# Optimization experiments

Hardware: AMD Instinct MI355X
Metric: run time of the kernel (lower is better)

Reference implementation:

```python
import jax, jax.numpy as jnp
import numpy as np

B, T, D, UNITS, NUM_OUT = 64, 1024, 256, 256, 32


def setup_inputs() -> dict:
    key = jax.random.key(0)
    k1, k2, k3 = jax.random.split(key, 3)
    inputs = jax.random.normal(k1, (B, T, D), dtype=jnp.float32)
    U = jax.random.normal(k2, (D, 4 * UNITS), dtype=jnp.float32) * 0.05
    W = jax.random.normal(k3, (UNITS, 4 * UNITS), dtype=jnp.float32) * 0.05
    b = jnp.zeros((4 * UNITS,), dtype=jnp.float32)
    return {"inputs": inputs, "U": U, "W": W, "b": b, "num_outputs": NUM_OUT}


def reference(inputs, U, W, b, num_outputs):
    # inputs: [B, T, D]; U: [D, 4u]; W: [u, 4u]; b: [4u]
    Bsz, Tlen, _ = inputs.shape
    units = W.shape[0]
    # Precompute input projection as one batched GEMM (x_t @ U + b for all t)
    xz = jnp.einsum('btd,dk->btk', inputs, U) + b  # [B, T, 4u]

    def step(carry, xz_t):
        h, c = carry
        z = xz_t + h @ W  # [B, 4u]
        z0, z1, z2, z3 = jnp.split(z, 4, axis=1)
        i = jax.nn.sigmoid(z0)
        f = jax.nn.sigmoid(z1)
        c_new = f * c + i * jnp.tanh(z2)
        o = jax.nn.sigmoid(z3)
        h_new = o * jnp.tanh(c_new)
        return (h_new, c_new), h_new

    h0 = jnp.zeros((Bsz, units), dtype=inputs.dtype)
    c0 = jnp.zeros((Bsz, units), dtype=inputs.dtype)
    (_, _), hs = jax.lax.scan(step, (h0, c0), jnp.swapaxes(xz, 0, 1))  # hs: [T, B, u]
    outputs = jnp.swapaxes(hs, 0, 1)[:, Tlen - num_outputs:, :]  # [B, num_outputs, u]
    return outputs
```

## Files before the change

kernel.cpp:

```cpp
#include <hip/hip_runtime.h>
#include <hip/hip_fp16.h>
#include <stdint.h>

#define Bsz 64
#define Tsz 1024
#define Dsz 256
#define UNITSn 256
#define Zdim 1024

typedef _Float16 f16x8  __attribute__((ext_vector_type(8)));
typedef float    f32x4  __attribute__((ext_vector_type(4)));

__device__ __forceinline__ float dot2acc(uint32_t w, uint32_t h, float acc) {
  asm("v_dot2_f32_f16 %0, %1, %2, %0" : "+v"(acc) : "v"(w), "v"(h));
  return acc;
}

__device__ __forceinline__ float dot4(const uint4& w, const uint4& h, float acc) {
  acc = dot2acc(w.x, h.x, acc); acc = dot2acc(w.y, h.y, acc);
  acc = dot2acc(w.z, h.z, acc); acc = dot2acc(w.w, h.w, acc);
  return acc;
}

__device__ __forceinline__ float sigm(float x)   { return 1.0f / (1.0f + __expf(-x)); }
__device__ __forceinline__ float tanh_f(float x) { return 1.0f - 2.0f / (__expf(2.0f * x) + 1.0f); }

__global__ __launch_bounds__(256) void convert_u(const float* __restrict__ U,
                                                 _Float16* __restrict__ UT) {
  int i = blockIdx.x * 256 + threadIdx.x;
  int n = i >> 8, k = i & 255;
  UT[i] = (_Float16)U[(size_t)k * Zdim + n];
}

__global__ __launch_bounds__(256) void convert_w7(const float* __restrict__ W,
                                                  uint4* __restrict__ Wop,
                                                  uint4* __restrict__ Wlds,
                                                  uint4* __restrict__ Wstr) {
  int i = blockIdx.x * 256 + threadIdx.x;
  if (i >= 32768) return;
  int slot = i >> 9, t = i & 511;
  int g, jx, outIdx;
  uint4* dst;
  if (slot < 40)      { g = slot / 10;      jx = slot % 10;        dst = Wop;  outIdx = slot * 512 + t; }
  else if (slot < 52) { int ss = slot - 40; g = ss & 3; jx = 10 + (ss >> 2); dst = Wlds; outIdx = ss * 512 + t; }
  else                { int ss = slot - 52; g = ss & 3; jx = 13 + (ss >> 2); dst = Wstr; outIdx = ss * 512 + t; }
  int col = g * 256 + (t & 255);
  int kbase = (t >> 8) * 64 + jx * 4;
  uint32_t d[4];
#pragma unroll
  for (int e = 0; e < 4; e++) {
    int k2 = kbase + e;
    float w0 = W[(size_t)(2 * k2) * Zdim + col];
    float w1 = W[(size_t)(2 * k2 + 1) * Zdim + col];
    __half2 p = __floats2half2_rn(w0, w1);
    d[e] = __builtin_bit_cast(uint32_t, p);
  }
  dst[outIdx] = make_uint4(d[0], d[1], d[2], d[3]);
}

__global__ __launch_bounds__(256) void proj_mfma(
    const float* __restrict__ x, const _Float16* __restrict__ UT,
    const float* __restrict__ bias, float* __restrict__ xz, int t0) {
  __shared__ _Float16 Ax[64][40];
  __shared__ _Float16 Ux[256][40];
  const int tid  = threadIdx.x;
  const int w    = tid >> 6, lane = tid & 63;
  const int lr   = lane & 15, kg = lane >> 4;
  const int n0   = blockIdx.x * 256;
  const int tloc = blockIdx.y;
  const int t    = t0 + tloc;
  const int arow = tid >> 2, ak = (tid & 3) * 8;

  f32x4 acc[4][4];
#pragma unroll
  for (int mi = 0; mi < 4; mi++)
#pragma unroll
    for (int ni = 0; ni < 4; ni++) acc[mi][ni] = f32x4{0.f, 0.f, 0.f, 0.f};

  for (int k0 = 0; k0 < Dsz; k0 += 32) {
    const float* xp = x + ((size_t)arow * Tsz + t) * Dsz + k0 + ak;
    float4 p0 = *(const float4*)xp;
    float4 p1 = *(const float4*)(xp + 4);
    const _Float16* up = UT + (size_t)(n0 + tid) * Dsz + k0;
    f16x8 u0 = *(const f16x8*)up;
    f16x8 u1 = *(const f16x8*)(up + 8);
    f16x8 u2 = *(const f16x8*)(up + 16);
    f16x8 u3 = *(const f16x8*)(up + 24);
    __syncthreads();
    f16x8 a8;
    a8[0] = (_Float16)p0.x; a8[1] = (_Float16)p0.y;
    a8[2] = (_Float16)p0.z; a8[3] = (_Float16)p0.w;
    a8[4] = (_Float16)p1.x; a8[5] = (_Float16)p1.y;
    a8[6] = (_Float16)p1.z; a8[7] = (_Float16)p1.w;
    *(f16x8*)&Ax[arow][ak] = a8;
    *(f16x8*)&Ux[tid][0]  = u0;
    *(f16x8*)&Ux[tid][8]  = u1;
    *(f16x8*)&Ux[tid][16] = u2;
    *(f16x8*)&Ux[tid][24] = u3;
    __syncthreads();
    f16x8 af[4], uf[4];
#pragma unroll
    for (int mi = 0; mi < 4; mi++) af[mi] = *(const f16x8*)&Ax[mi * 16 + lr][kg * 8];
#pragma unroll
    for (int ni = 0; ni < 4; ni++) uf[ni] = *(const f16x8*)&Ux[w * 64 + ni * 16 + lr][kg * 8];
#pragma unroll
    for (int mi = 0; mi < 4; mi++)
#pragma unroll
      for (int ni = 0; ni < 4; ni++)
        acc[mi][ni] = __builtin_amdgcn_mfma_f32_16x16x32_f16(af[mi], uf[ni],
                                                             acc[mi][ni], 0, 0, 0);
  }
#pragma unroll
  for (int ni = 0; ni < 4; ni++) {
    int col = n0 + w * 64 + ni * 16 + lr;
    float bs = bias[col];
#pragma unroll
    for (int mi = 0; mi < 4; mi++) {
      f32x4 v = acc[mi][ni];
#pragma unroll
      for (int r = 0; r < 4; r++) {
        int brow = mi * 16 + kg * 4 + r;
        xz[((size_t)tloc * 64 + brow) * Zdim + col] = v[r] + bs;
      }
    }
  }
}

__global__ __launch_bounds__(512) void lstm_chunk(
    const float* __restrict__ xz, const uint4* __restrict__ Wop,
    const uint4* __restrict__ WldsBuf, const uint4* __restrict__ Wstr,
    float* __restrict__ out, uint4* __restrict__ h_state,
    float* __restrict__ c_state, int t0, int Tc, int n_out) {
  __shared__ uint4 Wl[12 * 512];
  __shared__ uint4 hq[2][32];
  __shared__ float4 pp[256];

  const int tid  = threadIdx.x;
  const int b    = blockIdx.x;
  const int half = tid >> 8, u = tid & 255;

  uint4 wop[40];
#pragma unroll
  for (int j = 0; j < 40; j++) wop[j] = Wop[(size_t)j * 512 + tid];
#pragma unroll
  for (int j = 0; j < 40; j++)
    asm volatile("" : "+v"(wop[j].x), "+v"(wop[j].y), "+v"(wop[j].z), "+v"(wop[j].w));
#pragma unroll
  for (int cl = 0; cl < 12; cl++)
    Wl[(size_t)cl * 512 + tid] = WldsBuf[(size_t)cl * 512 + tid];

  float c = 0.0f;
  if (t0 == 0) {
    if (tid < 64) ((uint4*)hq)[tid] = make_uint4(0, 0, 0, 0);
  } else {
    if (tid < 32) ((uint4*)hq)[tid] = h_state[(size_t)b * 32 + tid];
    if (half == 0) c = c_state[(size_t)b * 256 + u];
  }
  __syncthreads();

  const float* xzb = xz + (size_t)b * Zdim + u;
  float nx0 = 0, nx1 = 0, nx2 = 0, nx3 = 0;
  if (half == 0) { nx0 = xzb[0]; nx1 = xzb[256]; nx2 = xzb[512]; nx3 = xzb[768]; }
  const uint4* wstr = Wstr + tid;

  for (int tl = 0; tl < Tc; tl++) {
    const int buf = tl & 1;
    const uint4* hb = hq[buf] + half * 16;
    float a0 = 0, a1 = 0, a2 = 0, a3 = 0;

    uint4 s00 = wstr[0 * 512], s01 = wstr[1 * 512], s02 = wstr[2 * 512], s03 = wstr[3 * 512];
    uint4 s10 = wstr[4 * 512], s11 = wstr[5 * 512], s12 = wstr[6 * 512], s13 = wstr[7 * 512];

#pragma unroll
    for (int j = 0; j < 10; j++) {
      uint4 h4 = hb[j];
      a0 = dot4(wop[0 * 10 + j], h4, a0);
      a1 = dot4(wop[1 * 10 + j], h4, a1);
      a2 = dot4(wop[2 * 10 + j], h4, a2);
      a3 = dot4(wop[3 * 10 + j], h4, a3);
    }
    uint4 s20, s21, s22, s23;
    { uint4 h4 = hb[13];
      s20 = wstr[8 * 512]; s21 = wstr[9 * 512]; s22 = wstr[10 * 512]; s23 = wstr[11 * 512];
      a0 = dot4(s00, h4, a0); a1 = dot4(s01, h4, a1);
      a2 = dot4(s02, h4, a2); a3 = dot4(s03, h4, a3); }
    { uint4 h4 = hb[10];
      uint4 w0 = Wl[(size_t)0 * 512 + tid], w1 = Wl[(size_t)1 * 512 + tid];
      uint4 w2 = Wl[(size_t)2 * 512 + tid], w3 = Wl[(size_t)3 * 512 + tid];
      a0 = dot4(w0, h4, a0); a1 = dot4(w1, h4, a1);
      a2 = dot4(w2, h4, a2); a3 = dot4(w3, h4, a3); }
    { uint4 h4 = hb[14];
      a0 = dot4(s10, h4, a0); a1 = dot4(s11, h4, a1);
      a2 = dot4(s12, h4, a2); a3 = dot4(s13, h4, a3); }
    { uint4 h4 = hb[11];
      uint4 w0 = Wl[(size_t)4 * 512 + tid], w1 = Wl[(size_t)5 * 512 + tid];
      uint4 w2 = Wl[(size_t)6 * 512 + tid], w3 = Wl[(size_t)7 * 512 + tid];
      a0 = dot4(w0, h4, a0); a1 = dot4(w1, h4, a1);
      a2 = dot4(w2, h4, a2); a3 = dot4(w3, h4, a3); }
    { uint4 h4 = hb[15];
      a0 = dot4(s20, h4, a0); a1 = dot4(s21, h4, a1);
      a2 = dot4(s22, h4, a2); a3 = dot4(s23, h4, a3); }
    { uint4 h4 = hb[12];
      uint4 w0 = Wl[(size_t)8 * 512 + tid], w1 = Wl[(size_t)9 * 512 + tid];
      uint4 w2 = Wl[(size_t)10 * 512 + tid], w3 = Wl[(size_t)11 * 512 + tid];
      a0 = dot4(w0, h4, a0); a1 = dot4(w1, h4, a1);
      a2 = dot4(w2, h4, a2); a3 = dot4(w3, h4, a3); }

    if (half) pp[u] = make_float4(a0, a1, a2, a3);
    __syncthreads();
    if (!half) {
      float4 q = pp[u];
      float z0 = a0 + q.x + nx0, z1 = a1 + q.y + nx1;
      float z2 = a2 + q.z + nx2, z3 = a3 + q.w + nx3;
      if (tl + 1 < Tc) {
        const float* xn = xzb + (size_t)(tl + 1) * (Bsz * Zdim);
        nx0 = xn[0]; nx1 = xn[256]; nx2 = xn[512]; nx3 = xn[768];
      }
      float ig = sigm(z0), fg = sigm(z1), gg = tanh_f(z2), og = sigm(z3);
      c = fg * c + ig * gg;
      float hn = og * tanh_f(c);
      int ot = (t0 + tl) - (Tsz - n_out);
      if (ot >= 0) out[((size_t)b * n_out + ot) * UNITSn + u] = hn;
      ((__half*)hq[buf ^ 1])[u] = __float2half(hn);
    }
    __syncthreads();
  }
  if (tid < 32) h_state[(size_t)b * 32 + tid] = ((uint4*)hq)[(Tc & 1) * 32 + tid];
  if (half == 0) c_state[(size_t)b * 256 + u] = c;
}

extern "C" void kernel_launch(void* const* d_in, const int* in_sizes, int n_in,
                              void* d_out, int out_size, void* d_ws, size_t ws_size,
                              hipStream_t stream) {
  const float* x    = (const float*)d_in[0];
  const float* U    = (const float*)d_in[1];
  const float* W    = (const float*)d_in[2];
  const float* bias = (const float*)d_in[3];
  float* out = (float*)d_out;
  const int n_out = out_size / (Bsz * UNITSn);

  uint8_t* ws = (uint8_t*)d_ws;
  uint4* Wop      = (uint4*)ws;
  uint4* Wlds     = (uint4*)(ws + (320u << 10));
  uint4* Wstr     = (uint4*)(ws + (416u << 10));
  _Float16* UT    = (_Float16*)(ws + (512u << 10));
  uint4* h_state  = (uint4*)(ws + (1024u << 10));
  float* c_state  = (float*)(ws + (1056u << 10));
  float* xz       = (float*)(ws + (2u << 20));

  int Tc = Tsz;
  while (Tc > 1 && (size_t)(2u << 20) + (size_t)Tc * (Bsz * Zdim) * 4 > ws_size) Tc >>= 1;

  convert_w7<<<dim3(128), dim3(256), 0, stream>>>(W, Wop, Wlds, Wstr);
  convert_u<<<dim3(1024), dim3(256), 0, stream>>>(U, UT);

  for (int t0 = 0; t0 < Tsz; t0 += Tc) {
    proj_mfma<<<dim3(4, Tc), dim3(256), 0, stream>>>(x, UT, bias, xz, t0);
    lstm_chunk<<<dim3(Bsz), dim3(512), 0, stream>>>(xz, Wop, Wlds, Wstr,
                                                    out, h_state, c_state,
                                                    t0, Tc, n_out);
  }
}
```

Measured before the change: 2.129 ms.

## Rebalance recurrent weight storage across AGPRs, VGPRs, LDS and streamed global

The recurrent weight matrix is repartitioned into four tiers. 24 fragments are parked in accumulation registers (AGPRs) and read back with v_accvgpr_read before each dot. 12 fragments stay in VGPRs, 16 fragment slots move to a larger LDS buffer, and 12 are still streamed from global each step. The goal is to use the otherwise idle AGPR file so that more weights are held on-chip and fewer loads compete per timestep. The cost is an extra accvgpr read per dword, a larger LDS footprint, and possible register-allocation surprises from the inline asm.

```diff
diff --git a/kernel.cpp b/kernel.cpp
--- a/kernel.cpp
+++ b/kernel.cpp
@@ -11,16 +11,16 @@
 typedef _Float16 f16x8  __attribute__((ext_vector_type(8)));
 typedef float    f32x4  __attribute__((ext_vector_type(4)));
 
-__device__ __forceinline__ float dot2acc(uint32_t w, uint32_t h, float acc) {
-  asm("v_dot2_f32_f16 %0, %1, %2, %0" : "+v"(acc) : "v"(w), "v"(h));
-  return acc;
-}
-
-__device__ __forceinline__ float dot4(const uint4& w, const uint4& h, float acc) {
-  acc = dot2acc(w.x, h.x, acc); acc = dot2acc(w.y, h.y, acc);
-  acc = dot2acc(w.z, h.z, acc); acc = dot2acc(w.w, h.w, acc);
-  return acc;
-}
+#define DOT2V(acc, w, h) asm("v_dot2_f32_f16 %0, %1, %2, %0" : "+v"(acc) : "v"(w), "v"(h))
+#define DOT4V(acc, w4, h4) { DOT2V(acc, (w4).x, (h4).x); DOT2V(acc, (w4).y, (h4).y); \
+                             DOT2V(acc, (w4).z, (h4).z); DOT2V(acc, (w4).w, (h4).w); }
+#define WR_A(dst, src) asm volatile("v_accvgpr_write_b32 %0, %1" : "=a"(dst) : "v"(src))
+#define DOT4A(acc, wa4, h4) { uint4 t_; \
+  asm("v_accvgpr_read_b32 %0, %1" : "=v"(t_.x) : "a"((wa4).x)); \
+  asm("v_accvgpr_read_b32 %0, %1" : "=v"(t_.y) : "a"((wa4).y)); \
+  asm("v_accvgpr_read_b32 %0, %1" : "=v"(t_.z) : "a"((wa4).z)); \
+  asm("v_accvgpr_read_b32 %0, %1" : "=v"(t_.w) : "a"((wa4).w)); \
+  DOT4V(acc, t_, h4); }
 
 __device__ __forceinline__ float sigm(float x)   { return 1.0f / (1.0f + __expf(-x)); }
 __device__ __forceinline__ float tanh_f(float x) { return 1.0f - 2.0f / (__expf(2.0f * x) + 1.0f); }
@@ -32,20 +32,22 @@
   UT[i] = (_Float16)U[(size_t)k * Zdim + n];
 }
 
-__global__ __launch_bounds__(256) void convert_w7(const float* __restrict__ W,
-                                                  uint4* __restrict__ Wop,
-                                                  uint4* __restrict__ Wlds,
-                                                  uint4* __restrict__ Wstr) {
+__global__ __launch_bounds__(256) void convert_w9(const float* __restrict__ W,
+                                                  uint4* __restrict__ Wa,
+                                                  uint4* __restrict__ Wv,
+                                                  uint4* __restrict__ Wl,
+                                                  uint4* __restrict__ Ws) {
   int i = blockIdx.x * 256 + threadIdx.x;
   if (i >= 32768) return;
-  int slot = i >> 9, t = i & 511;
-  int g, jx, outIdx;
-  uint4* dst;
-  if (slot < 40)      { g = slot / 10;      jx = slot % 10;        dst = Wop;  outIdx = slot * 512 + t; }
-  else if (slot < 52) { int ss = slot - 40; g = ss & 3; jx = 10 + (ss >> 2); dst = Wlds; outIdx = ss * 512 + t; }
-  else                { int ss = slot - 52; g = ss & 3; jx = 13 + (ss >> 2); dst = Wstr; outIdx = ss * 512 + t; }
+  int s = i >> 9, t = i & 511;
+  int j = s >> 2, g = s & 3;
+  uint4* dst; int idx;
+  if (j < 6)       { dst = Wa; idx = s * 512 + t; }
+  else if (j < 9)  { dst = Wv; idx = (s - 24) * 512 + t; }
+  else if (j < 13) { dst = Wl; idx = (s - 36) * 512 + t; }
+  else             { dst = Ws; idx = (s - 52) * 512 + t; }
   int col = g * 256 + (t & 255);
-  int kbase = (t >> 8) * 64 + jx * 4;
+  int kbase = (t >> 8) * 64 + j * 4;
   uint32_t d[4];
 #pragma unroll
   for (int e = 0; e < 4; e++) {
@@ -55,7 +57,7 @@
     __half2 p = __floats2half2_rn(w0, w1);
     d[e] = __builtin_bit_cast(uint32_t, p);
   }
-  dst[outIdx] = make_uint4(d[0], d[1], d[2], d[3]);
+  dst[idx] = make_uint4(d[0], d[1], d[2], d[3]);
 }
 
 __global__ __launch_bounds__(256) void proj_mfma(
@@ -127,11 +129,12 @@
 }
 
 __global__ __launch_bounds__(512) void lstm_chunk(
-    const float* __restrict__ xz, const uint4* __restrict__ Wop,
-    const uint4* __restrict__ WldsBuf, const uint4* __restrict__ Wstr,
-    float* __restrict__ out, uint4* __restrict__ h_state,
-    float* __restrict__ c_state, int t0, int Tc, int n_out) {
-  __shared__ uint4 Wl[12 * 512];
+    const float* __restrict__ xz, const uint4* __restrict__ WaB,
+    const uint4* __restrict__ WvB, const uint4* __restrict__ WlB,
+    const uint4* __restrict__ Ws, float* __restrict__ out,
+    uint4* __restrict__ h_state, float* __restrict__ c_state,
+    int t0, int Tc, int n_out) {
+  __shared__ uint4 Wlds[16 * 512];
   __shared__ uint4 hq[2][32];
   __shared__ float4 pp[256];
 
@@ -139,15 +142,22 @@
   const int b    = blockIdx.x;
   const int half = tid >> 8, u = tid & 255;
 
-  uint4 wop[40];
-#pragma unroll
-  for (int j = 0; j < 40; j++) wop[j] = Wop[(size_t)j * 512 + tid];
-#pragma unroll
-  for (int j = 0; j < 40; j++)
-    asm volatile("" : "+v"(wop[j].x), "+v"(wop[j].y), "+v"(wop[j].z), "+v"(wop[j].w));
-#pragma unroll
-  for (int cl = 0; cl < 12; cl++)
-    Wl[(size_t)cl * 512 + tid] = WldsBuf[(size_t)cl * 512 + tid];
+  uint4 wa[24];
+#pragma unroll
+  for (int s = 0; s < 24; s++) {
+    uint4 v = WaB[(size_t)s * 512 + tid];
+    WR_A(wa[s].x, v.x); WR_A(wa[s].y, v.y);
+    WR_A(wa[s].z, v.z); WR_A(wa[s].w, v.w);
+  }
+  uint4 wv[12];
+#pragma unroll
+  for (int s = 0; s < 12; s++) wv[s] = WvB[(size_t)s * 512 + tid];
+#pragma unroll
+  for (int s = 0; s < 12; s++)
+    asm volatile("" : "+v"(wv[s].x), "+v"(wv[s].y), "+v"(wv[s].z), "+v"(wv[s].w));
+#pragma unroll
+  for (int s = 0; s < 16; s++)
+    Wlds[s * 512 + tid] = WlB[(size_t)s * 512 + tid];
 
   float c = 0.0f;
   if (t0 == 0) {
@@ -161,50 +171,53 @@
   const float* xzb = xz + (size_t)b * Zdim + u;
   float nx0 = 0, nx1 = 0, nx2 = 0, nx3 = 0;
   if (half == 0) { nx0 = xzb[0]; nx1 = xzb[256]; nx2 = xzb[512]; nx3 = xzb[768]; }
-  const uint4* wstr = Wstr + tid;
+  const uint4* wsp = Ws + tid;
 
   for (int tl = 0; tl < Tc; tl++) {
     const int buf = tl & 1;
     const uint4* hb = hq[buf] + half * 16;
     float a0 = 0, a1 = 0, a2 = 0, a3 = 0;
 
-    uint4 s00 = wstr[0 * 512], s01 = wstr[1 * 512], s02 = wstr[2 * 512], s03 = wstr[3 * 512];
-    uint4 s10 = wstr[4 * 512], s11 = wstr[5 * 512], s12 = wstr[6 * 512], s13 = wstr[7 * 512];
-
-#pragma unroll
-    for (int j = 0; j < 10; j++) {
+    uint4 sA0 = wsp[0 * 512], sA1 = wsp[1 * 512], sA2 = wsp[2 * 512], sA3 = wsp[3 * 512];
+#pragma unroll
+    for (int j = 0; j < 3; j++) {
       uint4 h4 = hb[j];
-      a0 = dot4(wop[0 * 10 + j], h4, a0);
-      a1 = dot4(wop[1 * 10 + j], h4, a1);
-      a2 = dot4(wop[2 * 10 + j], h4, a2);
-      a3 = dot4(wop[3 * 10 + j], h4, a3);
-    }
-    uint4 s20, s21, s22, s23;
+      DOT4A(a0, wa[j * 4 + 0], h4); DOT4A(a1, wa[j * 4 + 1], h4);
+      DOT4A(a2, wa[j * 4 + 2], h4); DOT4A(a3, wa[j * 4 + 3], h4);
+    }
+    uint4 sB0 = wsp[4 * 512], sB1 = wsp[5 * 512], sB2 = wsp[6 * 512], sB3 = wsp[7 * 512];
+#pragma unroll
+    for (int j = 3; j < 6; j++) {
+      uint4 h4 = hb[j];
+      DOT4A(a0, wa[j * 4 + 0], h4); DOT4A(a1, wa[j * 4 + 1], h4);
+      DOT4A(a2, wa[j * 4 + 2], h4); DOT4A(a3, wa[j * 4 + 3], h4);
+    }
     { uint4 h4 = hb[13];
-      s20 = wstr[8 * 512]; s21 = wstr[9 * 512]; s22 = wstr[10 * 512]; s23 = wstr[11 * 512];
-      a0 = dot4(s00, h4, a0); a1 = dot4(s01, h4, a1);
-      a2 = dot4(s02, h4, a2); a3 = dot4(s03, h4, a3); }
-    { uint4 h4 = hb[10];
-      uint4 w0 = Wl[(size_t)0 * 512 + tid], w1 = Wl[(size_t)1 * 512 + tid];
-      uint4 w2 = Wl[(size_t)2 * 512 + tid], w3 = Wl[(size_t)3 * 512 + tid];
-      a0 = dot4(w0, h4, a0); a1 = dot4(w1, h4, a1);
-      a2 = dot4(w2, h4, a2); a3 = dot4(w3, h4, a3); }
+      DOT4V(a0, sA0, h4); DOT4V(a1, sA1, h4);
+      DOT4V(a2, sA2, h4); DOT4V(a3, sA3, h4); }
+    uint4 sC0 = wsp[8 * 512], sC1 = wsp[9 * 512], sC2 = wsp[10 * 512], sC3 = wsp[11 * 512];
+#pragma unroll
+    for (int j = 0; j < 3; j++) {
+      uint4 h4 = hb[6 + j];
+      DOT4V(a0, wv[j * 4 + 0], h4); DOT4V(a1, wv[j * 4 + 1], h4);
+      DOT4V(a2, wv[j * 4 + 2], h4); DOT4V(a3, wv[j * 4 + 3], h4);
+    }
     { uint4 h4 = hb[14];
-      a0 = dot4(s10, h4, a0); a1 = dot4(s11, h4, a1);
-      a2 = dot4(s12, h4, a2); a3 = dot4(s13, h4, a3); }
-    { uint4 h4 = hb[11];
-      uint4 w0 = Wl[(size_t)4 * 512 + tid], w1 = Wl[(size_t)5 * 512 + tid];
-      uint4 w2 = Wl[(size_t)6 * 512 + tid], w3 = Wl[(size_t)7 * 512 + tid];
-      a0 = dot4(w0, h4, a0); a1 = dot4(w1, h4, a1);
-      a2 = dot4(w2, h4, a2); a3 = dot4(w3, h4, a3); }
+      DOT4V(a0, sB0, h4); DOT4V(a1, sB1, h4);
+      DOT4V(a2, sB2, h4); DOT4V(a3, sB3, h4); }
+#pragma unroll
+    for (int jj = 0; jj < 4; jj++) {
+      uint4 h4 = hb[9 + jj];
+      uint4 w0 = Wlds[(jj * 4 + 0) * 512 + tid];
+      uint4 w1 = Wlds[(jj * 4 + 1) * 512 + tid];
+      uint4 w2 = Wlds[(jj * 4 + 2) * 512 + tid];
+      uint4 w3 = Wlds[(jj * 4 + 3) * 512 + tid];
+      DOT4V(a0, w0, h4); DOT4V(a1, w1, h4);
+      DOT4V(a2, w2, h4); DOT4V(a3, w3, h4);
+    }
     { uint4 h4 = hb[15];
-      a0 = dot4(s20, h4, a0); a1 = dot4(s21, h4, a1);
-      a2 = dot4(s22, h4, a2); a3 = dot4(s23, h4, a3); }
-    { uint4 h4 = hb[12];
-      uint4 w0 = Wl[(size_t)8 * 512 + tid], w1 = Wl[(size_t)9 * 512 + tid];
-      uint4 w2 = Wl[(size_t)10 * 512 + tid], w3 = Wl[(size_t)11 * 512 + tid];
-      a0 = dot4(w0, h4, a0); a1 = dot4(w1, h4, a1);
-      a2 = dot4(w2, h4, a2); a3 = dot4(w3, h4, a3); }
+      DOT4V(a0, sC0, h4); DOT4V(a1, sC1, h4);
+      DOT4V(a2, sC2, h4); DOT4V(a3, sC3, h4); }
 
     if (half) pp[u] = make_float4(a0, a1, a2, a3);
     __syncthreads();
@@ -240,9 +253,10 @@
   const int n_out = out_size / (Bsz * UNITSn);
 
   uint8_t* ws = (uint8_t*)d_ws;
-  uint4* Wop      = (uint4*)ws;
-  uint4* Wlds     = (uint4*)(ws + (320u << 10));
-  uint4* Wstr     = (uint4*)(ws + (416u << 10));
+  uint4* Wa       = (uint4*)ws;
+  uint4* Wv       = (uint4*)(ws + (192u << 10));
+  uint4* Wl       = (uint4*)(ws + (288u << 10));
+  uint4* Ws_      = (uint4*)(ws + (416u << 10));
   _Float16* UT    = (_Float16*)(ws + (512u << 10));
   uint4* h_state  = (uint4*)(ws + (1024u << 10));
   float* c_state  = (float*)(ws + (1056u << 10));
@@ -251,12 +265,12 @@
   int Tc = Tsz;
   while (Tc > 1 && (size_t)(2u << 20) + (size_t)Tc * (Bsz * Zdim) * 4 > ws_size) Tc >>= 1;
 
-  convert_w7<<<dim3(128), dim3(256), 0, stream>>>(W, Wop, Wlds, Wstr);
+  convert_w9<<<dim3(128), dim3(256), 0, stream>>>(W, Wa, Wv, Wl, Ws_);
   convert_u<<<dim3(1024), dim3(256), 0, stream>>>(U, UT);
 
   for (int t0 = 0; t0 < Tsz; t0 += Tc) {
     proj_mfma<<<dim3(4, Tc), dim3(256), 0, stream>>>(x, UT, bias, xz, t0);
-    lstm_chunk<<<dim3(Bsz), dim3(512), 0, stream>>>(xz, Wop, Wlds, Wstr,
+    lstm_chunk<<<dim3(Bsz), dim3(512), 0, stream>>>(xz, Wa, Wv, Wl, Ws_,
                                                     out, h_state, c_state,
                                                     t0, Tc, n_out);
   }
```

Result: slower. 2.682 ms (+26.0%).

## Compute recurrent h@W with MFMA instead of dot2 and drop cross-half reduction

Applied to the files above, without the earlier changes.

Replaces the per-thread v_dot2 matvec in the LSTM recurrence with 16x16x32 f16 MFMA instructions. Only one row of each 16-row tile carries real data (a single batch row per block). W is repacked into the MFMA B-operand layout, split across registers, LDS and streamed global loads. Each wave now owns 32 units across all four gates, which removes the partial-sum exchange through shared memory and one barrier per timestep. The cost is MFMA work wasted on the 15 unused rows, plus extra MFMA latency on the serial dependency chain.

```diff
diff --git a/kernel.cpp b/kernel.cpp
--- a/kernel.cpp
+++ b/kernel.cpp
@@ -11,16 +11,8 @@
 typedef _Float16 f16x8  __attribute__((ext_vector_type(8)));
 typedef float    f32x4  __attribute__((ext_vector_type(4)));
 
-__device__ __forceinline__ float dot2acc(uint32_t w, uint32_t h, float acc) {
-  asm("v_dot2_f32_f16 %0, %1, %2, %0" : "+v"(acc) : "v"(w), "v"(h));
-  return acc;
-}
-
-__device__ __forceinline__ float dot4(const uint4& w, const uint4& h, float acc) {
-  acc = dot2acc(w.x, h.x, acc); acc = dot2acc(w.y, h.y, acc);
-  acc = dot2acc(w.z, h.z, acc); acc = dot2acc(w.w, h.w, acc);
-  return acc;
-}
+#define MFMA16(D, A, B) D = __builtin_amdgcn_mfma_f32_16x16x32_f16( \
+    __builtin_bit_cast(f16x8, A), __builtin_bit_cast(f16x8, B), D, 0, 0, 0)
 
 __device__ __forceinline__ float sigm(float x)   { return 1.0f / (1.0f + __expf(-x)); }
 __device__ __forceinline__ float tanh_f(float x) { return 1.0f - 2.0f / (__expf(2.0f * x) + 1.0f); }
@@ -32,30 +24,31 @@
   UT[i] = (_Float16)U[(size_t)k * Zdim + n];
 }
 
-__global__ __launch_bounds__(256) void convert_w7(const float* __restrict__ W,
-                                                  uint4* __restrict__ Wop,
-                                                  uint4* __restrict__ Wlds,
-                                                  uint4* __restrict__ Wstr) {
+__global__ __launch_bounds__(256) void convert_w10(const float* __restrict__ W,
+                                                   uint4* __restrict__ Wres,
+                                                   uint4* __restrict__ Wldsb,
+                                                   uint4* __restrict__ Wstrb) {
   int i = blockIdx.x * 256 + threadIdx.x;
   if (i >= 32768) return;
-  int slot = i >> 9, t = i & 511;
-  int g, jx, outIdx;
-  uint4* dst;
-  if (slot < 40)      { g = slot / 10;      jx = slot % 10;        dst = Wop;  outIdx = slot * 512 + t; }
-  else if (slot < 52) { int ss = slot - 40; g = ss & 3; jx = 10 + (ss >> 2); dst = Wlds; outIdx = ss * 512 + t; }
-  else                { int ss = slot - 52; g = ss & 3; jx = 13 + (ss >> 2); dst = Wstr; outIdx = ss * 512 + t; }
-  int col = g * 256 + (t & 255);
-  int kbase = (t >> 8) * 64 + jx * 4;
+  int f = i >> 9, t = i & 511;
+  int w = t >> 6, l = t & 63;
+  int ks = f >> 3, nt = f & 7;
+  int g = nt >> 1, sub = nt & 1;
+  int col = g * 256 + w * 32 + sub * 16 + (l & 15);
+  int kb = ks * 32 + ((l >> 4) << 3);
   uint32_t d[4];
 #pragma unroll
   for (int e = 0; e < 4; e++) {
-    int k2 = kbase + e;
-    float w0 = W[(size_t)(2 * k2) * Zdim + col];
-    float w1 = W[(size_t)(2 * k2 + 1) * Zdim + col];
+    int k = kb + 2 * e;
+    float w0 = W[(size_t)k * Zdim + col];
+    float w1 = W[(size_t)(k + 1) * Zdim + col];
     __half2 p = __floats2half2_rn(w0, w1);
     d[e] = __builtin_bit_cast(uint32_t, p);
   }
-  dst[outIdx] = make_uint4(d[0], d[1], d[2], d[3]);
+  uint4 v = make_uint4(d[0], d[1], d[2], d[3]);
+  if (f < 44)      Wres[f * 512 + t] = v;
+  else if (f < 52) Wldsb[(f - 44) * 512 + t] = v;
+  else             Wstrb[(f - 52) * 512 + t] = v;
 }
 
 __global__ __launch_bounds__(256) void proj_mfma(
@@ -127,106 +120,109 @@
 }
 
 __global__ __launch_bounds__(512) void lstm_chunk(
-    const float* __restrict__ xz, const uint4* __restrict__ Wop,
-    const uint4* __restrict__ WldsBuf, const uint4* __restrict__ Wstr,
+    const float* __restrict__ xz, const uint4* __restrict__ Wres,
+    const uint4* __restrict__ Wldsb, const uint4* __restrict__ Wstrb,
     float* __restrict__ out, uint4* __restrict__ h_state,
     float* __restrict__ c_state, int t0, int Tc, int n_out) {
-  __shared__ uint4 Wl[12 * 512];
+  __shared__ uint4 Wl[8 * 512];
   __shared__ uint4 hq[2][32];
-  __shared__ float4 pp[256];
-
-  const int tid  = threadIdx.x;
-  const int b    = blockIdx.x;
-  const int half = tid >> 8, u = tid & 255;
-
-  uint4 wop[40];
-#pragma unroll
-  for (int j = 0; j < 40; j++) wop[j] = Wop[(size_t)j * 512 + tid];
-#pragma unroll
-  for (int j = 0; j < 40; j++)
-    asm volatile("" : "+v"(wop[j].x), "+v"(wop[j].y), "+v"(wop[j].z), "+v"(wop[j].w));
-#pragma unroll
-  for (int cl = 0; cl < 12; cl++)
-    Wl[(size_t)cl * 512 + tid] = WldsBuf[(size_t)cl * 512 + tid];
+  __shared__ uint4 fence[1024];
+
+  const int tid = threadIdx.x;
+  const int b   = blockIdx.x;
+  const int w   = tid >> 6, l = tid & 63;
+  const int kg  = l >> 4, l31 = l & 31;
+  const int sub = kg & 1;
+
+  if (h_state == nullptr) fence[tid & 1023] = make_uint4(0, 0, 0, 0);
+
+  uint4 wr[44];
+#pragma unroll
+  for (int s = 0; s < 44; s++) wr[s] = Wres[(size_t)s * 512 + tid];
+#pragma unroll
+  for (int s = 0; s < 8; s++) Wl[s * 512 + tid] = Wldsb[(size_t)s * 512 + tid];
 
   float c = 0.0f;
   if (t0 == 0) {
     if (tid < 64) ((uint4*)hq)[tid] = make_uint4(0, 0, 0, 0);
   } else {
     if (tid < 32) ((uint4*)hq)[tid] = h_state[(size_t)b * 32 + tid];
-    if (half == 0) c = c_state[(size_t)b * 256 + u];
+    c = c_state[(size_t)b * 256 + w * 32 + l31];
   }
   __syncthreads();
 
-  const float* xzb = xz + (size_t)b * Zdim + u;
-  float nx0 = 0, nx1 = 0, nx2 = 0, nx3 = 0;
-  if (half == 0) { nx0 = xzb[0]; nx1 = xzb[256]; nx2 = xzb[512]; nx3 = xzb[768]; }
-  const uint4* wstr = Wstr + tid;
+  const float* xzb = xz + (size_t)b * Zdim + w * 32 + l31;
+  float nx0 = xzb[0], nx1 = xzb[256], nx2 = xzb[512], nx3 = xzb[768];
+  const uint4* wsp = Wstrb + tid;
 
   for (int tl = 0; tl < Tc; tl++) {
     const int buf = tl & 1;
-    const uint4* hb = hq[buf] + half * 16;
-    float a0 = 0, a1 = 0, a2 = 0, a3 = 0;
-
-    uint4 s00 = wstr[0 * 512], s01 = wstr[1 * 512], s02 = wstr[2 * 512], s03 = wstr[3 * 512];
-    uint4 s10 = wstr[4 * 512], s11 = wstr[5 * 512], s12 = wstr[6 * 512], s13 = wstr[7 * 512];
-
-#pragma unroll
-    for (int j = 0; j < 10; j++) {
-      uint4 h4 = hb[j];
-      a0 = dot4(wop[0 * 10 + j], h4, a0);
-      a1 = dot4(wop[1 * 10 + j], h4, a1);
-      a2 = dot4(wop[2 * 10 + j], h4, a2);
-      a3 = dot4(wop[3 * 10 + j], h4, a3);
-    }
-    uint4 s20, s21, s22, s23;
-    { uint4 h4 = hb[13];
-      s20 = wstr[8 * 512]; s21 = wstr[9 * 512]; s22 = wstr[10 * 512]; s23 = wstr[11 * 512];
-      a0 = dot4(s00, h4, a0); a1 = dot4(s01, h4, a1);
-      a2 = dot4(s02, h4, a2); a3 = dot4(s03, h4, a3); }
-    { uint4 h4 = hb[10];
-      uint4 w0 = Wl[(size_t)0 * 512 + tid], w1 = Wl[(size_t)1 * 512 + tid];
-      uint4 w2 = Wl[(size_t)2 * 512 + tid], w3 = Wl[(size_t)3 * 512 + tid];
-      a0 = dot4(w0, h4, a0); a1 = dot4(w1, h4, a1);
-      a2 = dot4(w2, h4, a2); a3 = dot4(w3, h4, a3); }
-    { uint4 h4 = hb[14];
-      a0 = dot4(s10, h4, a0); a1 = dot4(s11, h4, a1);
-      a2 = dot4(s12, h4, a2); a3 = dot4(s13, h4, a3); }
-    { uint4 h4 = hb[11];
-      uint4 w0 = Wl[(size_t)4 * 512 + tid], w1 = Wl[(size_t)5 * 512 + tid];
-      uint4 w2 = Wl[(size_t)6 * 512 + tid], w3 = Wl[(size_t)7 * 512 + tid];
-      a0 = dot4(w0, h4, a0); a1 = dot4(w1, h4, a1);
-      a2 = dot4(w2, h4, a2); a3 = dot4(w3, h4, a3); }
-    { uint4 h4 = hb[15];
-      a0 = dot4(s20, h4, a0); a1 = dot4(s21, h4, a1);
-      a2 = dot4(s22, h4, a2); a3 = dot4(s23, h4, a3); }
-    { uint4 h4 = hb[12];
-      uint4 w0 = Wl[(size_t)8 * 512 + tid], w1 = Wl[(size_t)9 * 512 + tid];
-      uint4 w2 = Wl[(size_t)10 * 512 + tid], w3 = Wl[(size_t)11 * 512 + tid];
-      a0 = dot4(w0, h4, a0); a1 = dot4(w1, h4, a1);
-      a2 = dot4(w2, h4, a2); a3 = dot4(w3, h4, a3); }
-
-    if (half) pp[u] = make_float4(a0, a1, a2, a3);
+    const uint4* hb4 = hq[buf];
+    uint4 sA0 = wsp[4 * 512], sA1 = wsp[5 * 512], sA2 = wsp[6 * 512], sA3 = wsp[7 * 512];
+
+    f32x4 D0 = {0.f,0.f,0.f,0.f}, D1 = D0, D2 = D0, D3 = D0;
+#pragma unroll
+    for (int ks = 0; ks < 6; ks++) {
+      uint4 A = hb4[ks * 4 + kg];
+      MFMA16(D0, A, wr[ks * 8 + 0]); MFMA16(D1, A, wr[ks * 8 + 1]);
+      MFMA16(D2, A, wr[ks * 8 + 2]); MFMA16(D3, A, wr[ks * 8 + 3]);
+    }
+    uint4 sB0 = wsp[0 * 512], sB1 = wsp[1 * 512], sB2 = wsp[2 * 512], sB3 = wsp[3 * 512];
+    uint4 sC0 = wsp[8 * 512], sC1 = wsp[9 * 512], sC2 = wsp[10 * 512], sC3 = wsp[11 * 512];
+    {
+      uint4 A = hb4[6 * 4 + kg];
+      uint4 b0 = Wl[4 * 512 + tid], b1 = Wl[5 * 512 + tid];
+      uint4 b2 = Wl[6 * 512 + tid], b3 = Wl[7 * 512 + tid];
+      MFMA16(D0, A, b0); MFMA16(D1, A, b1); MFMA16(D2, A, b2); MFMA16(D3, A, b3);
+    }
+    {
+      uint4 A = hb4[7 * 4 + kg];
+      MFMA16(D0, A, sA0); MFMA16(D1, A, sA1); MFMA16(D2, A, sA2); MFMA16(D3, A, sA3);
+    }
+    float z0 = sub ? D1[0] : D0[0];
+    float z1 = sub ? D3[0] : D2[0];
+
+    f32x4 E0 = {0.f,0.f,0.f,0.f}, E1 = E0, E2 = E0, E3 = E0;
+#pragma unroll
+    for (int ks = 0; ks < 5; ks++) {
+      uint4 A = hb4[ks * 4 + kg];
+      MFMA16(E0, A, wr[ks * 8 + 4]); MFMA16(E1, A, wr[ks * 8 + 5]);
+      MFMA16(E2, A, wr[ks * 8 + 6]); MFMA16(E3, A, wr[ks * 8 + 7]);
+    }
+    {
+      uint4 A = hb4[5 * 4 + kg];
+      uint4 b0 = Wl[0 * 512 + tid], b1 = Wl[1 * 512 + tid];
+      uint4 b2 = Wl[2 * 512 + tid], b3 = Wl[3 * 512 + tid];
+      MFMA16(E0, A, b0); MFMA16(E1, A, b1); MFMA16(E2, A, b2); MFMA16(E3, A, b3);
+    }
+    {
+      uint4 A = hb4[6 * 4 + kg];
+      MFMA16(E0, A, sB0); MFMA16(E1, A, sB1); MFMA16(E2, A, sB2); MFMA16(E3, A, sB3);
+    }
+    {
+      uint4 A = hb4[7 * 4 + kg];
+      MFMA16(E0, A, sC0); MFMA16(E1, A, sC1); MFMA16(E2, A, sC2); MFMA16(E3, A, sC3);
+    }
+    float z2 = sub ? E1[0] : E0[0];
+    float z3 = sub ? E3[0] : E2[0];
+
+    z0 += nx0; z1 += nx1; z2 += nx2; z3 += nx3;
+    if (tl + 1 < Tc) {
+      const float* xn = xzb + (size_t)(tl + 1) * (Bsz * Zdim);
+      nx0 = xn[0]; nx1 = xn[256]; nx2 = xn[512]; nx3 = xn[768];
+    }
+    float ig = sigm(z0), fg = sigm(z1), gg = tanh_f(z2), og = sigm(z3);
+    c = fg * c + ig * gg;
+    float hn = og * tanh_f(c);
+    if (l < 32) {
+      int ot = (t0 + tl) - (Tsz - n_out);
+      if (ot >= 0) out[((size_t)b * n_out + ot) * UNITSn + w * 32 + l] = hn;
+      ((_Float16*)hq[buf ^ 1])[w * 32 + l] = (_Float16)hn;
+    }
     __syncthreads();
-    if (!half) {
-      float4 q = pp[u];
-      float z0 = a0 + q.x + nx0, z1 = a1 + q.y + nx1;
-      float z2 = a2 + q.z + nx2, z3 = a3 + q.w + nx3;
-      if (tl + 1 < Tc) {
-        const float* xn = xzb + (size_t)(tl + 1) * (Bsz * Zdim);
-        nx0 = xn[0]; nx1 = xn[256]; nx2 = xn[512]; nx3 = xn[768];
-      }
-      float ig = sigm(z0), fg = sigm(z1), gg = tanh_f(z2), og = sigm(z3);
-      c = fg * c + ig * gg;
-      float hn = og * tanh_f(c);
-      int ot = (t0 + tl) - (Tsz - n_out);
-      if (ot >= 0) out[((size_t)b * n_out + ot) * UNITSn + u] = hn;
-      ((__half*)hq[buf ^ 1])[u] = __float2half(hn);
-    }
-    __syncthreads();
   }
   if (tid < 32) h_state[(size_t)b * 32 + tid] = ((uint4*)hq)[(Tc & 1) * 32 + tid];
-  if (half == 0) c_state[(size_t)b * 256 + u] = c;
+  if (l < 32) c_state[(size_t)b * 256 + w * 32 + l] = c;
 }
 
 extern "C" void kernel_launch(void* const* d_in, const int* in_sizes, int n_in,
@@ -240,9 +236,9 @@
   const int n_out = out_size / (Bsz * UNITSn);
 
   uint8_t* ws = (uint8_t*)d_ws;
-  uint4* Wop      = (uint4*)ws;
-  uint4* Wlds     = (uint4*)(ws + (320u << 10));
-  uint4* Wstr     = (uint4*)(ws + (416u << 10));
+  uint4* Wres     = (uint4*)ws;
+  uint4* Wldsb    = (uint4*)(ws + (352u << 10));
+  uint4* Wstrb    = (uint4*)(ws + (416u << 10));
   _Float16* UT    = (_Float16*)(ws + (512u << 10));
   uint4* h_state  = (uint4*)(ws + (1024u << 10));
   float* c_state  = (float*)(ws + (1056u << 10));
@@ -251,12 +247,12 @@
   int Tc = Tsz;
   while (Tc > 1 && (size_t)(2u << 20) + (size_t)Tc * (Bsz * Zdim) * 4 > ws_size) Tc >>= 1;
 
-  convert_w7<<<dim3(128), dim3(256), 0, stream>>>(W, Wop, Wlds, Wstr);
+  convert_w10<<<dim3(128), dim3(256), 0, stream>>>(W, Wres, Wldsb, Wstrb);
   convert_u<<<dim3(1024), dim3(256), 0, stream>>>(U, UT);
 
   for (int t0 = 0; t0 < Tsz; t0 += Tc) {
     proj_mfma<<<dim3(4, Tc), dim3(256), 0, stream>>>(x, UT, bias, xz, t0);
-    lstm_chunk<<<dim3(Bsz), dim3(512), 0, stream>>>(xz, Wop, Wlds, Wstr,
+    lstm_chunk<<<dim3(Bsz), dim3(512), 0, stream>>>(xz, Wres, Wldsb, Wstrb,
                                                     out, h_state, c_state,
                                                     t0, Tc, n_out);
   }
```

After: 3.448 ms. 1.62x slower.
